# Performance work log

Hardware: AMD Instinct MI355X
Metric: run time of the kernel (lower is better)

Reference implementation:

```python
import jax, jax.numpy as jnp
import numpy as np

N = 12288          # neuron_count (nodes.shape[0])
R = 1024           # retina_output_size[1]
B = 32             # batch
N_LAYERS = 4       # CONNECTOME_LAYER_NUMBER
DENSITY = 0.05     # adjacency (connectome) sparsity
N_VISUAL = 2048    # neurons flagged 'visual'
N_RATIONAL = 64    # neurons flagged 'rational'


def setup_inputs() -> dict:
    key = jax.random.key(0)
    k_x, k_ret, k_sh, k_adj, k_rat, k_vis, k_ridx = jax.random.split(key, 7)

    x = jax.random.normal(k_x, (B, R), dtype=jnp.float32)

    # Retina layer: Linear(R -> N, bias=False); only rows at visual indices nonzero.
    vis_idx = jax.random.permutation(k_vis, N)[:N_VISUAL]
    vis_mask = jnp.zeros((N,), jnp.float32).at[vis_idx].set(1.0)
    W_retina = jax.random.normal(k_ret, (N, R), dtype=jnp.float32) * vis_mask[:, None]

    # Shared connectome weights: rand(N,N) masked by transposed adjacency != 0.
    adj = jax.random.bernoulli(k_adj, DENSITY, (N, N)).astype(jnp.float32)
    W_shared = jax.random.uniform(k_sh, (N, N), dtype=jnp.float32) * adj

    # Rational layer: Linear(N -> 2); only columns at rational indices nonzero.
    rat_idx = jax.random.permutation(k_ridx, N)[:N_RATIONAL]
    rat_mask = jnp.zeros((N,), jnp.float32).at[rat_idx].set(1.0)
    W_rational = jax.random.normal(k_rat, (2, N), dtype=jnp.float32) * rat_mask[None, :]

    return {"x": x, "W_retina": W_retina, "W_shared": W_shared,
            "W_rational": W_rational, "n_layers": N_LAYERS}


def reference(x, W_retina, W_shared, W_rational, n_layers):
    # retina: out = x @ W_retina^T   -> [B, N]
    out = jnp.einsum('br,nr->bn', x, W_retina)
    # repeated shared-weight Linear (bias-free): out = out @ W_shared^T
    for _ in range(n_layers):
        out = jnp.einsum('bn,mn->bm', out, W_shared)
    # rational readout: [B, 2]
    return jnp.einsum('bn,on->bo', out, W_rational)
```

## Files before the change

### kernel.cpp

```cpp
#include <hip/hip_runtime.h>
#include <cstddef>

#define NN 12288
#define RR 1024
#define BB 32

#define MSEGS 128
#define MROWS (NN / MSEGS)
#define JBLK (NN / 1024)
#define CAP 20
#define SEGB 4
#define HSEGS (MSEGS/SEGB)

#define PSEGS 256
#define PJ (NN / PSEGS)

typedef float vfloat4 __attribute__((ext_vector_type(4)));

__global__ __launch_bounds__(256) void build_kernel(
    const float* __restrict__ W, float* __restrict__ sval,
    unsigned char* __restrict__ scnt)
{
    __shared__ float slots[CAP * 1024];
    __shared__ int smax;

    const int t   = threadIdx.x;
    const int jb  = blockIdx.x;
    const int seg = blockIdx.y;
    const int j   = jb * 1024 + t * 4;
    const int m0  = seg * MROWS;

    if (t == 0) smax = 0;
    __syncthreads();

    const vfloat4* Wp = (const vfloat4*)(W + (size_t)m0 * NN + j);
    const int base = t * 4;

    int c0 = 0, c1 = 0, c2 = 0, c3 = 0;
    for (int i = 0; i < MROWS; i += 16) {
        vfloat4 w[16];
        #pragma unroll
        for (int u = 0; u < 16; ++u)
            w[u] = __builtin_nontemporal_load(Wp + (size_t)u * (NN / 4));
        Wp += 4 * NN;
        #pragma unroll
        for (int u = 0; u < 16; ++u) {
            const unsigned int li = (unsigned)(i + u);
            if (w[u].x != 0.f) { unsigned int b = __float_as_uint(w[u].x); if (c0 < CAP) slots[c0 * 1024 + base + 0] = __uint_as_float((b & 0xFFFFFF00u) | li); c0++; }
            if (w[u].y != 0.f) { unsigned int b = __float_as_uint(w[u].y); if (c1 < CAP) slots[c1 * 1024 + base + 1] = __uint_as_float((b & 0xFFFFFF00u) | li); c1++; }
            if (w[u].z != 0.f) { unsigned int b = __float_as_uint(w[u].z); if (c2 < CAP) slots[c2 * 1024 + base + 2] = __uint_as_float((b & 0xFFFFFF00u) | li); c2++; }
            if (w[u].w != 0.f) { unsigned int b = __float_as_uint(w[u].w); if (c3 < CAP) slots[c3 * 1024 + base + 3] = __uint_as_float((b & 0xFFFFFF00u) | li); c3++; }
        }
    }
    c0 = c0 < CAP ? c0 : CAP;  c1 = c1 < CAP ? c1 : CAP;
    c2 = c2 < CAP ? c2 : CAP;  c3 = c3 < CAP ? c3 : CAP;
    int cm = c0 > c1 ? c0 : c1; cm = cm > c2 ? cm : c2; cm = cm > c3 ? cm : c3;
    atomicMax(&smax, cm);
    __syncthreads();

    const int kmax = smax;
    float* dseg = sval + (size_t)seg * CAP * NN + j;
    for (int k = 0; k < kmax; ++k)
        *(float4*)(dseg + (size_t)k * NN) = *(const float4*)(slots + k * 1024 + base);

    uchar4 cn;
    cn.x = (unsigned char)c0; cn.y = (unsigned char)c1;
    cn.z = (unsigned char)c2; cn.w = (unsigned char)c3;
    *(uchar4*)(scnt + (size_t)seg * NN + j) = cn;
}

__global__ __launch_bounds__(256) void l1_kernel(
    const float* __restrict__ W, const float* __restrict__ Wrat,
    float* __restrict__ hout)
{
    __shared__ int knt;
    __shared__ int idxs[128];
    __shared__ float w0[128], w1[128];

    const int t  = threadIdx.x;
    const int j  = blockIdx.x * 1024 + t * 4;

    if (t == 0) knt = 0;
    __syncthreads();
    for (int m = t; m < NN; m += 256) {
        const float a = Wrat[m];
        const float b = Wrat[NN + m];
        if (a != 0.f || b != 0.f) {
            const int s = atomicAdd(&knt, 1);
            idxs[s] = m; w0[s] = a; w1[s] = b;
        }
    }
    __syncthreads();
    const int K = knt;

    float a00 = 0.f, a01 = 0.f, a02 = 0.f, a03 = 0.f;
    float a10 = 0.f, a11 = 0.f, a12 = 0.f, a13 = 0.f;
    for (int k = 0; k < K; ++k) {
        const float4 wv = *(const float4*)(W + (size_t)idxs[k] * NN + j);
        const float h0 = w0[k], h1 = w1[k];
        a00 = fmaf(h0, wv.x, a00); a01 = fmaf(h0, wv.y, a01);
        a02 = fmaf(h0, wv.z, a02); a03 = fmaf(h0, wv.w, a03);
        a10 = fmaf(h1, wv.x, a10); a11 = fmaf(h1, wv.y, a11);
        a12 = fmaf(h1, wv.z, a12); a13 = fmaf(h1, wv.w, a13);
    }
    float* d0 = hout + j;
    d0[0] = a00; d0[1] = a01; d0[2] = a02; d0[3] = a03;
    float* d1 = hout + NN + j;
    d1[0] = a10; d1[1] = a11; d1[2] = a12; d1[3] = a13;
}

__global__ __launch_bounds__(256) void sfold_kernel(
    const float* __restrict__ sval, const unsigned char* __restrict__ scnt,
    const float* __restrict__ hin, float* __restrict__ hpart)
{
    const int sb  = blockIdx.y;
    const int j   = blockIdx.x * 256 + threadIdx.x;
    const int m0  = sb * SEGB * MROWS;

    __shared__ float2 hs[SEGB * MROWS];
    for (int i = threadIdx.x; i < SEGB * MROWS; i += 256)
        hs[i] = make_float2(hin[m0 + i], hin[NN + m0 + i]);
    __syncthreads();

    float a0 = 0.f, a1 = 0.f;
    #pragma unroll
    for (int g = 0; g < SEGB; ++g) {
        const int seg = sb * SEGB + g;
        const int cnt = scnt[(size_t)seg * NN + j];
        const float* vp = sval + (size_t)seg * CAP * NN + j;
        const float2* hg = hs + g * MROWS;
        for (int k = 0; k < cnt; ++k) {
            const unsigned int b = __float_as_uint(vp[(size_t)k * NN]);
            const float v = __uint_as_float(b & 0xFFFFFF00u);
            const float2 h = hg[b & 0xFFu];
            a0 = fmaf(v, h.x, a0);
            a1 = fmaf(v, h.y, a1);
        }
    }
    hpart[((size_t)sb * 2) * NN + j]     = a0;
    hpart[((size_t)sb * 2 + 1) * NN + j] = a1;
}

__global__ __launch_bounds__(256) void reduce_h_kernel(
    const float* __restrict__ hpart, float* __restrict__ hout)
{
    const int idx = blockIdx.x * 256 + threadIdx.x;
    float s = 0.f;
    for (int sb = 0; sb < HSEGS; ++sb)
        s += hpart[(size_t)sb * 2 * NN + idx];
    hout[idx] = s;
}

__global__ __launch_bounds__(256) void retina_fold_kernel(
    const float* __restrict__ Wret, const float* __restrict__ h,
    float* __restrict__ ppart)
{
    const int seg = blockIdx.x;
    const int t   = threadIdx.x;
    const int j0  = seg * PJ;

    __shared__ float h0s[PJ];
    __shared__ float h1s[PJ];
    if (t < PJ) {
        h0s[t] = h[j0 + t];
        h1s[t] = h[NN + j0 + t];
    }
    __syncthreads();

    const int r = t * 4;
    float a00 = 0.f, a01 = 0.f, a02 = 0.f, a03 = 0.f;
    float a10 = 0.f, a11 = 0.f, a12 = 0.f, a13 = 0.f;

    const float4* Wp = (const float4*)(Wret + (size_t)j0 * RR + r);
    #pragma unroll 8
    for (int i = 0; i < PJ; ++i) {
        const float4 w = *Wp;
        Wp += RR / 4;
        const float h0 = h0s[i];
        const float h1 = h1s[i];
        a00 = fmaf(h0, w.x, a00); a01 = fmaf(h0, w.y, a01);
        a02 = fmaf(h0, w.z, a02); a03 = fmaf(h0, w.w, a03);
        a10 = fmaf(h1, w.x, a10); a11 = fmaf(h1, w.y, a11);
        a12 = fmaf(h1, w.z, a12); a13 = fmaf(h1, w.w, a13);
    }

    float* d0 = ppart + ((size_t)seg * 2) * RR + r;
    d0[0] = a00; d0[1] = a01; d0[2] = a02; d0[3] = a03;
    float* d1 = d0 + RR;
    d1[0] = a10; d1[1] = a11; d1[2] = a12; d1[3] = a13;
}

__global__ __launch_bounds__(256) void reduce_p_kernel(
    const float* __restrict__ ppart, float* __restrict__ p)
{
    const int idx = blockIdx.x * 256 + threadIdx.x;
    float s = 0.f;
    for (int seg = 0; seg < PSEGS; ++seg)
        s += ppart[(size_t)seg * 2 * RR + idx];
    p[idx] = s;
}

__global__ __launch_bounds__(64) void final_kernel(
    const float* __restrict__ x, const float* __restrict__ p,
    float* __restrict__ out)
{
    const int t = threadIdx.x;
    const int b = t >> 1;
    const int o = t & 1;
    const float4* xp = (const float4*)(x + (size_t)b * RR);
    const float4* pp = (const float4*)(p + (size_t)o * RR);
    float s = 0.f;
    for (int i = 0; i < RR / 4; ++i) {
        const float4 xv = xp[i];
        const float4 pv = pp[i];
        s = fmaf(xv.x, pv.x, s);
        s = fmaf(xv.y, pv.y, s);
        s = fmaf(xv.z, pv.z, s);
        s = fmaf(xv.w, pv.w, s);
    }
    out[b * 2 + o] = s;
}

extern "C" void kernel_launch(void* const* d_in, const int* in_sizes, int n_in,
                              void* d_out, int out_size, void* d_ws, size_t ws_size,
                              hipStream_t stream) {
    const float* x    = (const float*)d_in[0];
    const float* Wret = (const float*)d_in[1];
    const float* Ws   = (const float*)d_in[2];
    const float* Wrat = (const float*)d_in[3];

    char* ws = (char*)d_ws;
    float*         sval  = (float*)(ws + 0);
    unsigned char* scnt  = (unsigned char*)(ws + 125829120);
    float*         hpart = (float*)(ws + 127401984);
    float*         ppart = (float*)(ws + 130547712);
    float*         hA    = (float*)(ws + 132644864);
    float*         hB    = (float*)(ws + 132743168);
    float*         p     = (float*)(ws + 132841472);

    const dim3 buildGrid(JBLK, MSEGS);
    const dim3 sfoldGrid(NN / 256, HSEGS);

    build_kernel<<<buildGrid, 256, 0, stream>>>(Ws, sval, scnt);

    l1_kernel<<<JBLK, 256, 0, stream>>>(Ws, Wrat, hA);

    sfold_kernel<<<sfoldGrid, 256, 0, stream>>>(sval, scnt, hA, hpart);
    reduce_h_kernel<<<(2 * NN) / 256, 256, 0, stream>>>(hpart, hB);

    sfold_kernel<<<sfoldGrid, 256, 0, stream>>>(sval, scnt, hB, hpart);
    reduce_h_kernel<<<(2 * NN) / 256, 256, 0, stream>>>(hpart, hA);

    sfold_kernel<<<sfoldGrid, 256, 0, stream>>>(sval, scnt, hA, hpart);
    reduce_h_kernel<<<(2 * NN) / 256, 256, 0, stream>>>(hpart, hB);

    retina_fold_kernel<<<PSEGS, 256, 0, stream>>>(Wret, hB, ppart);
    reduce_p_kernel<<<(2 * RR) / 256, 256, 0, stream>>>(ppart, p);

    final_kernel<<<1, 64, 0, stream>>>(x, p, (float*)d_out);
}
```

Measured before the change: 938.3 us.

## Fuse first sparse propagation step into the compaction build kernel

Result: faster. 910.1 us (-3.0%).

```diff
diff --git a/kernel.cpp b/kernel.cpp
--- a/kernel.cpp
+++ b/kernel.cpp
@@ -8,7 +8,7 @@
 #define MSEGS 128
 #define MROWS (NN / MSEGS)
 #define JBLK (NN / 1024)
-#define CAP 20
+#define CAP 19
 #define SEGB 4
 #define HSEGS (MSEGS/SEGB)
 
@@ -17,11 +17,53 @@
 
 typedef float vfloat4 __attribute__((ext_vector_type(4)));
 
-__global__ __launch_bounds__(256) void build_kernel(
-    const float* __restrict__ W, float* __restrict__ sval,
-    unsigned char* __restrict__ scnt)
+__global__ __launch_bounds__(256) void l1_kernel(
+    const float* __restrict__ W, const float* __restrict__ Wrat,
+    float* __restrict__ hout)
+{
+    __shared__ int knt;
+    __shared__ int idxs[128];
+    __shared__ float w0[128], w1[128];
+
+    const int t  = threadIdx.x;
+    const int j  = blockIdx.x * 1024 + t * 4;
+
+    if (t == 0) knt = 0;
+    __syncthreads();
+    for (int m = t; m < NN; m += 256) {
+        const float a = Wrat[m];
+        const float b = Wrat[NN + m];
+        if (a != 0.f || b != 0.f) {
+            const int s = atomicAdd(&knt, 1);
+            idxs[s] = m; w0[s] = a; w1[s] = b;
+        }
+    }
+    __syncthreads();
+    const int K = knt;
+
+    float a00 = 0.f, a01 = 0.f, a02 = 0.f, a03 = 0.f;
+    float a10 = 0.f, a11 = 0.f, a12 = 0.f, a13 = 0.f;
+    for (int k = 0; k < K; ++k) {
+        const float4 wv = *(const float4*)(W + (size_t)idxs[k] * NN + j);
+        const float h0 = w0[k], h1 = w1[k];
+        a00 = fmaf(h0, wv.x, a00); a01 = fmaf(h0, wv.y, a01);
+        a02 = fmaf(h0, wv.z, a02); a03 = fmaf(h0, wv.w, a03);
+        a10 = fmaf(h1, wv.x, a10); a11 = fmaf(h1, wv.y, a11);
+        a12 = fmaf(h1, wv.z, a12); a13 = fmaf(h1, wv.w, a13);
+    }
+    float* d0 = hout + j;
+    d0[0] = a00; d0[1] = a01; d0[2] = a02; d0[3] = a03;
+    float* d1 = hout + NN + j;
+    d1[0] = a10; d1[1] = a11; d1[2] = a12; d1[3] = a13;
+}
+
+__global__ __launch_bounds__(256) void build_fold2_kernel(
+    const float* __restrict__ W, const float* __restrict__ h1,
+    float* __restrict__ sval, unsigned char* __restrict__ scnt,
+    float* __restrict__ hpart2)
 {
     __shared__ float slots[CAP * 1024];
+    __shared__ float2 hs[MROWS];
     __shared__ int smax;
 
     const int t   = threadIdx.x;
@@ -31,10 +73,14 @@
     const int m0  = seg * MROWS;
 
     if (t == 0) smax = 0;
+    if (t < MROWS) hs[t] = make_float2(h1[m0 + t], h1[NN + m0 + t]);
     __syncthreads();
 
     const vfloat4* Wp = (const vfloat4*)(W + (size_t)m0 * NN + j);
     const int base = t * 4;
+
+    float a00 = 0.f, a01 = 0.f, a02 = 0.f, a03 = 0.f;
+    float a10 = 0.f, a11 = 0.f, a12 = 0.f, a13 = 0.f;
 
     int c0 = 0, c1 = 0, c2 = 0, c3 = 0;
     for (int i = 0; i < MROWS; i += 16) {
@@ -46,18 +92,44 @@
         #pragma unroll
         for (int u = 0; u < 16; ++u) {
             const unsigned int li = (unsigned)(i + u);
-            if (w[u].x != 0.f) { unsigned int b = __float_as_uint(w[u].x); if (c0 < CAP) slots[c0 * 1024 + base + 0] = __uint_as_float((b & 0xFFFFFF00u) | li); c0++; }
-            if (w[u].y != 0.f) { unsigned int b = __float_as_uint(w[u].y); if (c1 < CAP) slots[c1 * 1024 + base + 1] = __uint_as_float((b & 0xFFFFFF00u) | li); c1++; }
-            if (w[u].z != 0.f) { unsigned int b = __float_as_uint(w[u].z); if (c2 < CAP) slots[c2 * 1024 + base + 2] = __uint_as_float((b & 0xFFFFFF00u) | li); c2++; }
-            if (w[u].w != 0.f) { unsigned int b = __float_as_uint(w[u].w); if (c3 < CAP) slots[c3 * 1024 + base + 3] = __uint_as_float((b & 0xFFFFFF00u) | li); c3++; }
+            const float2 h = hs[i + u];
+            if (w[u].x != 0.f) {
+                unsigned int b = __float_as_uint(w[u].x);
+                if (c0 < CAP) slots[c0 * 1024 + base + 0] = __uint_as_float((b & 0xFFFFFF00u) | li);
+                c0++;
+                a00 = fmaf(w[u].x, h.x, a00); a10 = fmaf(w[u].x, h.y, a10);
+            }
+            if (w[u].y != 0.f) {
+                unsigned int b = __float_as_uint(w[u].y);
+                if (c1 < CAP) slots[c1 * 1024 + base + 1] = __uint_as_float((b & 0xFFFFFF00u) | li);
+                c1++;
+                a01 = fmaf(w[u].y, h.x, a01); a11 = fmaf(w[u].y, h.y, a11);
+            }
+            if (w[u].z != 0.f) {
+                unsigned int b = __float_as_uint(w[u].z);
+                if (c2 < CAP) slots[c2 * 1024 + base + 2] = __uint_as_float((b & 0xFFFFFF00u) | li);
+                c2++;
+                a02 = fmaf(w[u].z, h.x, a02); a12 = fmaf(w[u].z, h.y, a12);
+            }
+            if (w[u].w != 0.f) {
+                unsigned int b = __float_as_uint(w[u].w);
+                if (c3 < CAP) slots[c3 * 1024 + base + 3] = __uint_as_float((b & 0xFFFFFF00u) | li);
+                c3++;
+                a03 = fmaf(w[u].w, h.x, a03); a13 = fmaf(w[u].w, h.y, a13);
+            }
         }
     }
     c0 = c0 < CAP ? c0 : CAP;  c1 = c1 < CAP ? c1 : CAP;
     c2 = c2 < CAP ? c2 : CAP;  c3 = c3 < CAP ? c3 : CAP;
     int cm = c0 > c1 ? c0 : c1; cm = cm > c2 ? cm : c2; cm = cm > c3 ? cm : c3;
     atomicMax(&smax, cm);
-    __syncthreads();
-
+
+    float* d0 = hpart2 + ((size_t)seg * 2) * NN + j;
+    d0[0] = a00; d0[1] = a01; d0[2] = a02; d0[3] = a03;
+    float* d1 = d0 + NN;
+    d1[0] = a10; d1[1] = a11; d1[2] = a12; d1[3] = a13;
+
+    __syncthreads();
     const int kmax = smax;
     float* dseg = sval + (size_t)seg * CAP * NN + j;
     for (int k = 0; k < kmax; ++k)
@@ -67,46 +139,6 @@
     cn.x = (unsigned char)c0; cn.y = (unsigned char)c1;
     cn.z = (unsigned char)c2; cn.w = (unsigned char)c3;
     *(uchar4*)(scnt + (size_t)seg * NN + j) = cn;
-}
-
-__global__ __launch_bounds__(256) void l1_kernel(
-    const float* __restrict__ W, const float* __restrict__ Wrat,
-    float* __restrict__ hout)
-{
-    __shared__ int knt;
-    __shared__ int idxs[128];
-    __shared__ float w0[128], w1[128];
-
-    const int t  = threadIdx.x;
-    const int j  = blockIdx.x * 1024 + t * 4;
-
-    if (t == 0) knt = 0;
-    __syncthreads();
-    for (int m = t; m < NN; m += 256) {
-        const float a = Wrat[m];
-        const float b = Wrat[NN + m];
-        if (a != 0.f || b != 0.f) {
-            const int s = atomicAdd(&knt, 1);
-            idxs[s] = m; w0[s] = a; w1[s] = b;
-        }
-    }
-    __syncthreads();
-    const int K = knt;
-
-    float a00 = 0.f, a01 = 0.f, a02 = 0.f, a03 = 0.f;
-    float a10 = 0.f, a11 = 0.f, a12 = 0.f, a13 = 0.f;
-    for (int k = 0; k < K; ++k) {
-        const float4 wv = *(const float4*)(W + (size_t)idxs[k] * NN + j);
-        const float h0 = w0[k], h1 = w1[k];
-        a00 = fmaf(h0, wv.x, a00); a01 = fmaf(h0, wv.y, a01);
-        a02 = fmaf(h0, wv.z, a02); a03 = fmaf(h0, wv.w, a03);
-        a10 = fmaf(h1, wv.x, a10); a11 = fmaf(h1, wv.y, a11);
-        a12 = fmaf(h1, wv.z, a12); a13 = fmaf(h1, wv.w, a13);
-    }
-    float* d0 = hout + j;
-    d0[0] = a00; d0[1] = a01; d0[2] = a02; d0[3] = a03;
-    float* d1 = hout + NN + j;
-    d1[0] = a10; d1[1] = a11; d1[2] = a12; d1[3] = a13;
 }
 
 __global__ __launch_bounds__(256) void sfold_kernel(
@@ -141,12 +173,13 @@
     hpart[((size_t)sb * 2 + 1) * NN + j] = a1;
 }
 
+template<int NPART>
 __global__ __launch_bounds__(256) void reduce_h_kernel(
     const float* __restrict__ hpart, float* __restrict__ hout)
 {
     const int idx = blockIdx.x * 256 + threadIdx.x;
     float s = 0.f;
-    for (int sb = 0; sb < HSEGS; ++sb)
+    for (int sb = 0; sb < NPART; ++sb)
         s += hpart[(size_t)sb * 2 * NN + idx];
     hout[idx] = s;
 }
@@ -231,28 +264,26 @@
 
     char* ws = (char*)d_ws;
     float*         sval  = (float*)(ws + 0);
-    unsigned char* scnt  = (unsigned char*)(ws + 125829120);
-    float*         hpart = (float*)(ws + 127401984);
-    float*         ppart = (float*)(ws + 130547712);
-    float*         hA    = (float*)(ws + 132644864);
-    float*         hB    = (float*)(ws + 132743168);
-    float*         p     = (float*)(ws + 132841472);
+    unsigned char* scnt  = (unsigned char*)(ws + 119537664);
+    float*         hpart = (float*)(ws + 121110528);
+    float*         ppart = (float*)(ws + 133693440);
+    float*         hA    = (float*)(ws + 135790592);
+    float*         hB    = (float*)(ws + 135888896);
+    float*         p     = (float*)(ws + 135987200);
 
     const dim3 buildGrid(JBLK, MSEGS);
     const dim3 sfoldGrid(NN / 256, HSEGS);
 
-    build_kernel<<<buildGrid, 256, 0, stream>>>(Ws, sval, scnt);
-
     l1_kernel<<<JBLK, 256, 0, stream>>>(Ws, Wrat, hA);
 
+    build_fold2_kernel<<<buildGrid, 256, 0, stream>>>(Ws, hA, sval, scnt, hpart);
+    reduce_h_kernel<MSEGS><<<(2 * NN) / 256, 256, 0, stream>>>(hpart, hB);
+
+    sfold_kernel<<<sfoldGrid, 256, 0, stream>>>(sval, scnt, hB, hpart);
+    reduce_h_kernel<HSEGS><<<(2 * NN) / 256, 256, 0, stream>>>(hpart, hA);
+
     sfold_kernel<<<sfoldGrid, 256, 0, stream>>>(sval, scnt, hA, hpart);
-    reduce_h_kernel<<<(2 * NN) / 256, 256, 0, stream>>>(hpart, hB);
-
-    sfold_kernel<<<sfoldGrid, 256, 0, stream>>>(sval, scnt, hB, hpart);
-    reduce_h_kernel<<<(2 * NN) / 256, 256, 0, stream>>>(hpart, hA);
-
-    sfold_kernel<<<sfoldGrid, 256, 0, stream>>>(sval, scnt, hA, hpart);
-    reduce_h_kernel<<<(2 * NN) / 256, 256, 0, stream>>>(hpart, hB);
+    reduce_h_kernel<HSEGS><<<(2 * NN) / 256, 256, 0, stream>>>(hpart, hB);
 
     retina_fold_kernel<<<PSEGS, 256, 0, stream>>>(Wret, hB, ppart);
     reduce_p_kernel<<<(2 * RR) / 256, 256, 0, stream>>>(ppart, p);
```
